# Performance work log

Measured on AMD Instinct MI355X. Metric: run time of the kernel, lower is better.

Reference implementation:

```python
import jax, jax.numpy as jnp
from jax import lax
import numpy as np
import math

MAXV = 127.0  # 2**(8-1)-1, signed int8 narrow range

def setup_inputs() -> dict:
    key = jax.random.key(0)
    kx, kw, kb = jax.random.split(key, 3)
    B, Cin, H, W = 32, 128, 56, 56
    Cout, K = 256, 3
    x = jax.random.normal(kx, (B, Cin, H, W), dtype=jnp.float32)
    # kaiming_uniform_(a=sqrt(5)) -> bound = sqrt(6 / ((1+5) * fan_in)) = 1/sqrt(fan_in)
    fan_in = Cin * K * K
    bound = 1.0 / math.sqrt(fan_in)
    weight = jax.random.uniform(kw, (Cout, Cin, K, K), dtype=jnp.float32,
                                minval=-bound, maxval=bound)
    bias = jax.random.uniform(kb, (Cout,), dtype=jnp.float32,
                              minval=-bound, maxval=bound)
    return {"x": x, "weight": weight, "bias": bias}

def _quantize_i8(t):
    """Max-calibrated signed 8-bit quantization (fake_quant=False -> integer output)."""
    amax = jnp.max(jnp.abs(t))
    scale = MAXV / amax
    q = jnp.clip(jnp.round(t * scale), -MAXV, MAXV).astype(jnp.int8)
    return q, scale

def reference(x, weight, bias):
    # quantize activations and weights to int8
    qx, sx = _quantize_i8(x)
    qw, sw = _quantize_i8(weight)
    # exact int8 conv with int32 accumulation (systolic exact path), stride=1, pad=1
    out_i32 = lax.conv_general_dilated(
        qx, qw,
        window_strides=(1, 1),
        padding=((1, 1), (1, 1)),
        dimension_numbers=("NCHW", "OIHW", "NCHW"),
        preferred_element_type=jnp.int32,
    )
    # dequantize and add bias
    out = out_i32.astype(jnp.float32) / (sx * sw)
    return out + bias[None, :, None, None]
```

## Files before the change

kernel.cpp:

```cpp
#include <hip/hip_runtime.h>


#define B_    32
#define CIN   128
#define H_    56
#define W_    56
#define COUT  256
#define HP    58
#define WP    58
#define HWP   (H_*W_)
#define NPIX  (B_*HWP)
#define NCHUNK 18
#define WCHUNK 16384

typedef int int4v __attribute__((ext_vector_type(4)));

__device__ __forceinline__ void gld_lds16(const void* g, void* l) {
    __builtin_amdgcn_global_load_lds(
        (const __attribute__((address_space(1))) unsigned int*)g,
        (__attribute__((address_space(3))) unsigned int*)l, 16, 0, 0);
}

__global__ __launch_bounds__(256) void amax_kernel(const float4* __restrict__ x, long n4x,
                                                   const float4* __restrict__ wt, long n4w,
                                                   unsigned* __restrict__ scales) {
    const float4* p; long n4; unsigned* slot; long start, stride;
    if (blockIdx.x < 2048) {
        p = x; n4 = n4x; slot = scales;
        start = (long)blockIdx.x * 256 + threadIdx.x; stride = 2048L * 256;
    } else {
        p = wt; n4 = n4w; slot = scales + 1;
        start = (long)(blockIdx.x - 2048) * 256 + threadIdx.x; stride = 128L * 256;
    }
    float m = 0.f;
    for (long i = start; i < n4; i += stride) {
        float4 v = p[i];
        m = fmaxf(m, fmaxf(fmaxf(fabsf(v.x), fabsf(v.y)), fmaxf(fabsf(v.z), fabsf(v.w))));
    }
    __shared__ float red[256];
    red[threadIdx.x] = m; __syncthreads();
    for (int s = 128; s > 0; s >>= 1) {
        if (threadIdx.x < s) red[threadIdx.x] = fmaxf(red[threadIdx.x], red[threadIdx.x + s]);
        __syncthreads();
    }
    if (threadIdx.x == 0) atomicMax(slot, __float_as_uint(red[0]));
}

__global__ __launch_bounds__(256) void quant_x_kernel(const float* __restrict__ x,
        const unsigned* __restrict__ scales, signed char* __restrict__ xq) {
    const int bh = blockIdx.x;
    const int b = bh / H_, h = bh % H_;
    const float sx = 127.0f / __uint_as_float(scales[0]);
    __shared__ int ldsq[W_ * 33];
    const int tid = threadIdx.x;

    int4 z; z.x = 0; z.y = 0; z.z = 0; z.w = 0;
    int4* prow = (int4*)(xq + ((long)b * HP + h + 1) * WP * CIN);
    if (tid < 8) prow[tid] = z;
    else if (tid < 16) prow[456 + tid - 8] = z;
    if (h == 0) {
        int4* r0 = (int4*)(xq + (long)b * HP * WP * CIN);
        for (int i = tid; i < 464; i += 256) r0[i] = z;
    } else if (h == H_ - 1) {
        int4* rt = (int4*)(xq + ((long)b * HP + 57) * WP * CIN);
        for (int i = tid; i < 464; i += 256) rt[i] = z;
    }

    const int w = tid & 63;
    const int chi = tid >> 6;
    if (w < W_) {
        const float* xb = x + (long)b * CIN * HWP + h * W_ + w;
#pragma unroll
        for (int it = 0; it < 8; ++it) {
            const int c4 = it * 4 + chi;
            int pk = 0;
#pragma unroll
            for (int u = 0; u < 4; ++u) {
                float v = xb[(long)(c4 * 4 + u) * HWP];
                float q = fminf(127.f, fmaxf(-127.f, rintf(v * sx)));
                pk |= ((int)q & 0xff) << (u * 8);
            }
            ldsq[w * 33 + c4] = pk;
        }
    }
    __syncthreads();
    int4* dst = (int4*)(xq + (((long)b * HP + h + 1) * WP + 1) * CIN);
    for (int idx = tid; idx < W_ * 8; idx += 256) {
        const int ww = idx >> 3, c16 = idx & 7;
        int4 v;
        v.x = ldsq[ww * 33 + c16 * 4 + 0];
        v.y = ldsq[ww * 33 + c16 * 4 + 1];
        v.z = ldsq[ww * 33 + c16 * 4 + 2];
        v.w = ldsq[ww * 33 + c16 * 4 + 3];
        dst[ww * 8 + c16] = v;
    }
}

__global__ __launch_bounds__(256) void quant_w_kernel(const float* __restrict__ wt,
        const unsigned* __restrict__ scales, signed char* __restrict__ wq) {
    const int id = blockIdx.x * 256 + threadIdx.x;
    if (id >= COUT * 9 * 32) return;
    const float sw = 127.0f / __uint_as_float(scales[1]);
    const int co = id / 288;
    const int r  = id % 288;
    const int t  = r / 32;
    const int c4 = r % 32;
    int pk = 0;
#pragma unroll
    for (int u = 0; u < 4; ++u) {
        float v = wt[(co * CIN + c4 * 4 + u) * 9 + t];
        float q = fminf(127.f, fmaxf(-127.f, rintf(v * sw)));
        pk |= ((int)q & 0xff) << (u * 8);
    }
    const int k = t * CIN + c4 * 4;
    const int chunk = k >> 6;
    const int o = k & 63;
    *(int*)(wq + (long)chunk * WCHUNK + (co >> 7) * 8192 +
            (o >> 4) * 2048 + (co & 127) * 16 + (o & 15)) = pk;
}

__global__ __launch_bounds__(256, 3) void conv_kernel(
        const signed char* __restrict__ xq, const signed char* __restrict__ wq,
        const float* __restrict__ bias, const unsigned* __restrict__ scales,
        float* __restrict__ out) {
    __shared__ signed char smem[24576];

    const int tid = threadIdx.x;
    const int lane = tid & 63;
    const int wv = tid >> 6;
    const int ln = lane & 15;
    const int g  = lane >> 4;

    const int wco2 = wv >> 1;
    const int wpx2 = wv & 1;

    const int bid = blockIdx.x;
    const int wg  = (bid & 7) * 196 + (bid >> 3);
    const int pxt = wg >> 1;
    const int cot = wg & 1;
    const int px_blk = pxt * 128;
    const int cotoff = cot * 8192;

    const int aoff0 = wv * 1024 + lane * 16;
    const int aoff1 = aoff0 + 4096;

    int voff[4];
#pragma unroll
    for (int j = 0; j < 4; ++j) {
        const int pxs = px_blk + wpx2 * 64 + j * 16 + ln;
        const int bS = pxs / HWP, hwS = pxs % HWP;
        const int hS = hwS / W_, wS = hwS % W_;
        voff[j] = ((bS * HP + hS) * WP + wS) * CIN + g * 16;
    }
    const int voff0 = voff[0], voff1 = voff[1], voff2 = voff[2], voff3 = voff[3];

#define STAGE_A(c) { const int bf_ = (c) % 3; \
    gld_lds16(wq + (c) * WCHUNK + cotoff + aoff0, &smem[bf_ * 8192 + aoff0]); \
    gld_lds16(wq + (c) * WCHUNK + cotoff + aoff1, &smem[bf_ * 8192 + aoff1]); }

#define LOADB(c, BN) { const int tap_ = (c) >> 1; \
    const signed char* p_ = xq + ((tap_ / 3) * WP + (tap_ % 3)) * CIN + ((c) & 1) * 64; \
    BN##0 = *(const int4v*)(p_ + voff0); BN##1 = *(const int4v*)(p_ + voff1); \
    BN##2 = *(const int4v*)(p_ + voff2); BN##3 = *(const int4v*)(p_ + voff3); }

#define LDA_(i) (*(const int4v*)&smem[buf * 8192 + g * 2048 + (wco2 * 64 + (i) * 16 + ln) * 16])
#define MM(i, j, A, Bv) acc[i][j] = __builtin_amdgcn_mfma_i32_16x16x64_i8(A, Bv, acc[i][j], 0, 0, 0)

#define CHUNK(c, VM, BC, BN) { \
    const int buf = (c) % 3; \
    asm volatile("s_waitcnt vmcnt(" #VM ")\n\ts_barrier" ::: "memory"); \
    if ((c) + 2 < NCHUNK) STAGE_A((c) + 2); \
    __builtin_amdgcn_sched_barrier(0);   \
    if ((c) + 1 < NCHUNK) LOADB((c) + 1, BN); \
    int4v Af0 = LDA_(0), Af1 = LDA_(1), Af2 = LDA_(2), Af3 = LDA_(3); \
    __builtin_amdgcn_s_setprio(1); \
    MM(0, 0, Af0, BC##0); MM(0, 1, Af0, BC##1); MM(0, 2, Af0, BC##2); MM(0, 3, Af0, BC##3); \
    MM(1, 0, Af1, BC##0); MM(1, 1, Af1, BC##1); MM(1, 2, Af1, BC##2); MM(1, 3, Af1, BC##3); \
    MM(2, 0, Af2, BC##0); MM(2, 1, Af2, BC##1); MM(2, 2, Af2, BC##2); MM(2, 3, Af2, BC##3); \
    MM(3, 0, Af3, BC##0); MM(3, 1, Af3, BC##1); MM(3, 2, Af3, BC##2); MM(3, 3, Af3, BC##3); \
    __builtin_amdgcn_s_setprio(0); }

    int4v acc[4][4] = {};
    int4v Ba0, Ba1, Ba2, Ba3, Bb0, Bb1, Bb2, Bb3;
    STAGE_A(0);
    __builtin_amdgcn_sched_barrier(0);
    STAGE_A(1);
    __builtin_amdgcn_sched_barrier(0);
    LOADB(0, Ba);
    CHUNK(0,  6, Ba, Bb) CHUNK(1,  6, Bb, Ba) CHUNK(2,  6, Ba, Bb) CHUNK(3,  6, Bb, Ba)
    CHUNK(4,  6, Ba, Bb) CHUNK(5,  6, Bb, Ba) CHUNK(6,  6, Ba, Bb) CHUNK(7,  6, Bb, Ba)
    CHUNK(8,  6, Ba, Bb) CHUNK(9,  6, Bb, Ba) CHUNK(10, 6, Ba, Bb) CHUNK(11, 6, Bb, Ba)
    CHUNK(12, 6, Ba, Bb) CHUNK(13, 6, Bb, Ba) CHUNK(14, 6, Ba, Bb) CHUNK(15, 6, Bb, Ba)
    CHUNK(16, 6, Ba, Bb) CHUNK(17, 4, Bb, Ba)
#undef CHUNK
#undef MM
#undef LDA_
#undef LOADB
#undef STAGE_A

    const float ax = __uint_as_float(scales[0]);
    const float aw = __uint_as_float(scales[1]);
    const float inv = 1.0f / ((127.0f / ax) * (127.0f / aw));

    __syncthreads();
    float* ldsT = (float*)smem;

    const int c4 = tid & 31;
    const int rsel = tid >> 5;
    const int px4 = px_blk + c4 * 4;
    const int bb = px4 / HWP, hw = px4 - bb * HWP;
    float* outb = out + ((long)bb * COUT + cot * 128) * HWP + hw;

#pragma unroll
    for (int rnd = 0; rnd < 4; ++rnd) {
        if (wco2 == (rnd >> 1)) {
#pragma unroll
            for (int ii = 0; ii < 2; ++ii) {
                const int i = (rnd & 1) * 2 + ii;
#pragma unroll
                for (int r = 0; r < 4; ++r) {
                    const int cl = ii * 16 + g * 4 + r;
#pragma unroll
                    for (int j = 0; j < 4; ++j)
                        ldsT[cl * 130 + wpx2 * 64 + j * 16 + ln] = (float)acc[i][j][r] * inv;
                }
            }
        }
        __syncthreads();
#pragma unroll
        for (int rr = 0; rr < 4; ++rr) {
            const int row = rr * 8 + rsel;
            const int co = rnd * 32 + row;
            float4 v = *(float4*)&ldsT[row * 130 + c4 * 4];
            const float bsv = bias[cot * 128 + co];
            v.x += bsv; v.y += bsv; v.z += bsv; v.w += bsv;
            *(float4*)&outb[(long)co * HWP] = v;
        }
        if (rnd < 3) __syncthreads();
    }
}

extern "C" void kernel_launch(void* const* d_in, const int* in_sizes, int n_in,
                              void* d_out, int out_size, void* d_ws, size_t ws_size,
                              hipStream_t stream) {
    const float* x  = (const float*)d_in[0];
    const float* wt = (const float*)d_in[1];
    const float* bs = (const float*)d_in[2];
    float* out = (float*)d_out;

    unsigned* scales = (unsigned*)d_ws;
    const size_t XQ_OFF   = 256;
    const size_t XQ_BYTES = (size_t)B_ * HP * WP * CIN;
    signed char* xq = (signed char*)d_ws + XQ_OFF;
    signed char* wq = xq + XQ_BYTES;

    hipMemsetAsync(d_ws, 0, 8, stream);

    const long n4x = (long)B_ * CIN * H_ * W_ / 4;
    const long n4w = (long)COUT * CIN * 9 / 4;
    amax_kernel<<<2176, 256, 0, stream>>>((const float4*)x, n4x, (const float4*)wt, n4w, scales);

    quant_x_kernel<<<B_ * H_, 256, 0, stream>>>(x, scales, xq);
    quant_w_kernel<<<(COUT * 9 * 32 + 255) / 256, 256, 0, stream>>>(wt, scales, wq);

    conv_kernel<<<2 * NPIX / 128, 256, 0, stream>>>(xq, wq, bs, scales, out);
}
```

Before: 240.6 us.

## Stage activation tiles into LDS via async global_load_lds alongside weights

Activation (B operand) fragments are no longer loaded straight from global memory into registers. They are now staged into a triple-buffered LDS region with direct global-to-LDS loads, in the same pipeline as the weight tiles, and read back from LDS per chunk. The goal is to cut duplicated global activation loads across the two waves that share pixels, coalesce the fetches, and free the registers used for double-buffering B. In exchange, LDS use doubles to 48KB, which may limit occupancy at the launch bound of 3 blocks, and each chunk adds LDS reads.

```diff
diff --git a/kernel.cpp b/kernel.cpp
--- a/kernel.cpp
+++ b/kernel.cpp
@@ -123,7 +123,7 @@
         const signed char* __restrict__ xq, const signed char* __restrict__ wq,
         const float* __restrict__ bias, const unsigned* __restrict__ scales,
         float* __restrict__ out) {
-    __shared__ signed char smem[24576];
+    __shared__ signed char smem[49152];
 
     const int tid = threadIdx.x;
     const int lane = tid & 63;
@@ -144,59 +144,52 @@
     const int aoff0 = wv * 1024 + lane * 16;
     const int aoff1 = aoff0 + 4096;
 
-    int voff[4];
-#pragma unroll
-    for (int j = 0; j < 4; ++j) {
-        const int pxs = px_blk + wpx2 * 64 + j * 16 + ln;
-        const int bS = pxs / HWP, hwS = pxs % HWP;
-        const int hS = hwS / W_, wS = hwS % W_;
-        voff[j] = ((bS * HP + hS) * WP + wS) * CIN + g * 16;
-    }
-    const int voff0 = voff[0], voff1 = voff[1], voff2 = voff[2], voff3 = voff[3];
-
-#define STAGE_A(c) { const int bf_ = (c) % 3; \
+    const int px0 = px_blk + lane;
+    const int b0 = px0 / HWP, hw0 = px0 % HWP;
+    const int voffB0 = ((b0 * HP + hw0 / W_) * WP + hw0 % W_) * CIN + wv * 16;
+    const int px1 = px_blk + 64 + lane;
+    const int b1 = px1 / HWP, hw1 = px1 % HWP;
+    const int voffB1 = ((b1 * HP + hw1 / W_) * WP + hw1 % W_) * CIN + wv * 16;
+    const int ldsB0 = wv * 2048 + lane * 16;
+    const int ldsB1 = ldsB0 + 1024;
+
+#define STAGE(c) { const int bf_ = (c) % 3; \
     gld_lds16(wq + (c) * WCHUNK + cotoff + aoff0, &smem[bf_ * 8192 + aoff0]); \
-    gld_lds16(wq + (c) * WCHUNK + cotoff + aoff1, &smem[bf_ * 8192 + aoff1]); }
-
-#define LOADB(c, BN) { const int tap_ = (c) >> 1; \
-    const signed char* p_ = xq + ((tap_ / 3) * WP + (tap_ % 3)) * CIN + ((c) & 1) * 64; \
-    BN##0 = *(const int4v*)(p_ + voff0); BN##1 = *(const int4v*)(p_ + voff1); \
-    BN##2 = *(const int4v*)(p_ + voff2); BN##3 = *(const int4v*)(p_ + voff3); }
+    gld_lds16(wq + (c) * WCHUNK + cotoff + aoff1, &smem[bf_ * 8192 + aoff1]); \
+    const int tap_ = (c) >> 1; \
+    const int toff_ = ((tap_ / 3) * WP + (tap_ % 3)) * CIN + ((c) & 1) * 64; \
+    gld_lds16(xq + toff_ + voffB0, &smem[24576 + bf_ * 8192 + ldsB0]); \
+    gld_lds16(xq + toff_ + voffB1, &smem[24576 + bf_ * 8192 + ldsB1]); }
 
 #define LDA_(i) (*(const int4v*)&smem[buf * 8192 + g * 2048 + (wco2 * 64 + (i) * 16 + ln) * 16])
+#define LDB_(j) (*(const int4v*)&smem[24576 + buf * 8192 + g * 2048 + (wpx2 * 64 + (j) * 16 + ln) * 16])
 #define MM(i, j, A, Bv) acc[i][j] = __builtin_amdgcn_mfma_i32_16x16x64_i8(A, Bv, acc[i][j], 0, 0, 0)
 
-#define CHUNK(c, VM, BC, BN) { \
+#define CHUNK(c, VM) { \
     const int buf = (c) % 3; \
     asm volatile("s_waitcnt vmcnt(" #VM ")\n\ts_barrier" ::: "memory"); \
-    if ((c) + 2 < NCHUNK) STAGE_A((c) + 2); \
-    __builtin_amdgcn_sched_barrier(0);   \
-    if ((c) + 1 < NCHUNK) LOADB((c) + 1, BN); \
+    if ((c) + 2 < NCHUNK) STAGE((c) + 2); \
+    int4v Bf0 = LDB_(0), Bf1 = LDB_(1), Bf2 = LDB_(2), Bf3 = LDB_(3); \
     int4v Af0 = LDA_(0), Af1 = LDA_(1), Af2 = LDA_(2), Af3 = LDA_(3); \
     __builtin_amdgcn_s_setprio(1); \
-    MM(0, 0, Af0, BC##0); MM(0, 1, Af0, BC##1); MM(0, 2, Af0, BC##2); MM(0, 3, Af0, BC##3); \
-    MM(1, 0, Af1, BC##0); MM(1, 1, Af1, BC##1); MM(1, 2, Af1, BC##2); MM(1, 3, Af1, BC##3); \
-    MM(2, 0, Af2, BC##0); MM(2, 1, Af2, BC##1); MM(2, 2, Af2, BC##2); MM(2, 3, Af2, BC##3); \
-    MM(3, 0, Af3, BC##0); MM(3, 1, Af3, BC##1); MM(3, 2, Af3, BC##2); MM(3, 3, Af3, BC##3); \
+    MM(0, 0, Af0, Bf0); MM(0, 1, Af0, Bf1); MM(0, 2, Af0, Bf2); MM(0, 3, Af0, Bf3); \
+    MM(1, 0, Af1, Bf0); MM(1, 1, Af1, Bf1); MM(1, 2, Af1, Bf2); MM(1, 3, Af1, Bf3); \
+    MM(2, 0, Af2, Bf0); MM(2, 1, Af2, Bf1); MM(2, 2, Af2, Bf2); MM(2, 3, Af2, Bf3); \
+    MM(3, 0, Af3, Bf0); MM(3, 1, Af3, Bf1); MM(3, 2, Af3, Bf2); MM(3, 3, Af3, Bf3); \
     __builtin_amdgcn_s_setprio(0); }
 
     int4v acc[4][4] = {};
-    int4v Ba0, Ba1, Ba2, Ba3, Bb0, Bb1, Bb2, Bb3;
-    STAGE_A(0);
+    STAGE(0);
     __builtin_amdgcn_sched_barrier(0);
-    STAGE_A(1);
-    __builtin_amdgcn_sched_barrier(0);
-    LOADB(0, Ba);
-    CHUNK(0,  6, Ba, Bb) CHUNK(1,  6, Bb, Ba) CHUNK(2,  6, Ba, Bb) CHUNK(3,  6, Bb, Ba)
-    CHUNK(4,  6, Ba, Bb) CHUNK(5,  6, Bb, Ba) CHUNK(6,  6, Ba, Bb) CHUNK(7,  6, Bb, Ba)
-    CHUNK(8,  6, Ba, Bb) CHUNK(9,  6, Bb, Ba) CHUNK(10, 6, Ba, Bb) CHUNK(11, 6, Bb, Ba)
-    CHUNK(12, 6, Ba, Bb) CHUNK(13, 6, Bb, Ba) CHUNK(14, 6, Ba, Bb) CHUNK(15, 6, Bb, Ba)
-    CHUNK(16, 6, Ba, Bb) CHUNK(17, 4, Bb, Ba)
+    STAGE(1);
+    CHUNK(0,  4) CHUNK(1,  4) CHUNK(2,  4) CHUNK(3,  4) CHUNK(4,  4) CHUNK(5,  4)
+    CHUNK(6,  4) CHUNK(7,  4) CHUNK(8,  4) CHUNK(9,  4) CHUNK(10, 4) CHUNK(11, 4)
+    CHUNK(12, 4) CHUNK(13, 4) CHUNK(14, 4) CHUNK(15, 4) CHUNK(16, 4) CHUNK(17, 0)
 #undef CHUNK
 #undef MM
 #undef LDA_
-#undef LOADB
-#undef STAGE_A
+#undef LDB_
+#undef STAGE
 
     const float ax = __uint_as_float(scales[0]);
     const float aw = __uint_as_float(scales[1]);
```

Measured after the change: 214.5 us. 10.9% less time.

## Stage padded input row window in LDS and reuse across all conv taps

Applied to the files above, without the earlier changes.

Each block now covers two full output rows of one image (112 pixels) instead of an arbitrary 128-pixel span. Its padded 4x58x128 int8 input window is loaded into LDS once, and B fragments for all 9 taps are read from LDS rather than re-fetched from global memory per chunk. Waves are re-split so each covers 32 output channels by 112 pixels with a 2x7 accumulator tile, and the epilogue is adapted to row-aligned stores. The cost is a larger LDS footprint (about 54KB per block, which puts pressure on the 3-blocks-per-CU target) and an unpipelined prologue load of the window.

```diff
diff --git a/kernel.cpp b/kernel.cpp
--- a/kernel.cpp
+++ b/kernel.cpp
@@ -12,6 +12,8 @@
 #define NPIX  (B_*HWP)
 #define NCHUNK 18
 #define WCHUNK 16384
+#define BWIN  24576
+#define GSTR  3712
 
 typedef int int4v __attribute__((ext_vector_type(4)));
 
@@ -123,7 +125,7 @@
         const signed char* __restrict__ xq, const signed char* __restrict__ wq,
         const float* __restrict__ bias, const unsigned* __restrict__ scales,
         float* __restrict__ out) {
-    __shared__ signed char smem[24576];
+    __shared__ signed char smem[54272];
 
     const int tid = threadIdx.x;
     const int lane = tid & 63;
@@ -131,71 +133,76 @@
     const int ln = lane & 15;
     const int g  = lane >> 4;
 
-    const int wco2 = wv >> 1;
-    const int wpx2 = wv & 1;
-
     const int bid = blockIdx.x;
-    const int wg  = (bid & 7) * 196 + (bid >> 3);
+    const int wg  = (bid & 7) * 224 + (bid >> 3);
     const int pxt = wg >> 1;
     const int cot = wg & 1;
-    const int px_blk = pxt * 128;
+    const int px_blk = pxt * 112;
     const int cotoff = cot * 8192;
+
+    const int b0 = pxt / 28;
+    const int h0 = (pxt % 28) * 2;
 
     const int aoff0 = wv * 1024 + lane * 16;
     const int aoff1 = aoff0 + 4096;
 
-    int voff[4];
-#pragma unroll
-    for (int j = 0; j < 4; ++j) {
-        const int pxs = px_blk + wpx2 * 64 + j * 16 + ln;
-        const int bS = pxs / HWP, hwS = pxs % HWP;
-        const int hS = hwS / W_, wS = hwS % W_;
-        voff[j] = ((bS * HP + hS) * WP + wS) * CIN + g * 16;
-    }
-    const int voff0 = voff[0], voff1 = voff[1], voff2 = voff[2], voff3 = voff[3];
+    int px58v[7];
+#pragma unroll
+    for (int j = 0; j < 7; ++j) {
+        const int pl = j * 16 + ln;
+        px58v[j] = pl + (pl >= 56 ? 2 : 0);
+    }
+
+    const signed char* win = xq + (long)(b0 * HP + h0) * WP * CIN;
+    int4v wbuf[8];
+#pragma unroll
+    for (int k = 0; k < 8; ++k) {
+        const int u = tid + k * 256;
+        if (u < 1856) wbuf[k] = *(const int4v*)(win + u * 16);
+    }
+#pragma unroll
+    for (int k = 0; k < 8; ++k) {
+        const int u = tid + k * 256;
+        if (u < 1856)
+            *(int4v*)&smem[BWIN + (u & 7) * GSTR + (u >> 3) * 16] = wbuf[k];
+    }
 
 #define STAGE_A(c) { const int bf_ = (c) % 3; \
     gld_lds16(wq + (c) * WCHUNK + cotoff + aoff0, &smem[bf_ * 8192 + aoff0]); \
     gld_lds16(wq + (c) * WCHUNK + cotoff + aoff1, &smem[bf_ * 8192 + aoff1]); }
 
-#define LOADB(c, BN) { const int tap_ = (c) >> 1; \
-    const signed char* p_ = xq + ((tap_ / 3) * WP + (tap_ % 3)) * CIN + ((c) & 1) * 64; \
-    BN##0 = *(const int4v*)(p_ + voff0); BN##1 = *(const int4v*)(p_ + voff1); \
-    BN##2 = *(const int4v*)(p_ + voff2); BN##3 = *(const int4v*)(p_ + voff3); }
-
-#define LDA_(i) (*(const int4v*)&smem[buf * 8192 + g * 2048 + (wco2 * 64 + (i) * 16 + ln) * 16])
+    STAGE_A(0);
+    STAGE_A(1);
+    asm volatile("s_waitcnt lgkmcnt(0)" ::: "memory");
+
+#define TAP58(c) ((((c) >> 1) / 3) * 58 + (((c) >> 1) % 3))
+#define LDA_(i) (*(const int4v*)&smem[buf * 8192 + g * 2048 + (wv * 32 + (i) * 16 + ln) * 16])
+#define LDB_(c, j) (*(const int4v*)&smem[BWIN + (((c) & 1) * 4 + g) * GSTR + (px58v[j] + TAP58(c)) * 16])
 #define MM(i, j, A, Bv) acc[i][j] = __builtin_amdgcn_mfma_i32_16x16x64_i8(A, Bv, acc[i][j], 0, 0, 0)
 
-#define CHUNK(c, VM, BC, BN) { \
+#define CHUNK(c, VM) { \
     const int buf = (c) % 3; \
     asm volatile("s_waitcnt vmcnt(" #VM ")\n\ts_barrier" ::: "memory"); \
     if ((c) + 2 < NCHUNK) STAGE_A((c) + 2); \
-    __builtin_amdgcn_sched_barrier(0);   \
-    if ((c) + 1 < NCHUNK) LOADB((c) + 1, BN); \
-    int4v Af0 = LDA_(0), Af1 = LDA_(1), Af2 = LDA_(2), Af3 = LDA_(3); \
+    int4v Bf0 = LDB_(c, 0), Bf1 = LDB_(c, 1), Bf2 = LDB_(c, 2), Bf3 = LDB_(c, 3); \
+    int4v Bf4 = LDB_(c, 4), Bf5 = LDB_(c, 5), Bf6 = LDB_(c, 6); \
+    int4v Af0 = LDA_(0), Af1 = LDA_(1); \
     __builtin_amdgcn_s_setprio(1); \
-    MM(0, 0, Af0, BC##0); MM(0, 1, Af0, BC##1); MM(0, 2, Af0, BC##2); MM(0, 3, Af0, BC##3); \
-    MM(1, 0, Af1, BC##0); MM(1, 1, Af1, BC##1); MM(1, 2, Af1, BC##2); MM(1, 3, Af1, BC##3); \
-    MM(2, 0, Af2, BC##0); MM(2, 1, Af2, BC##1); MM(2, 2, Af2, BC##2); MM(2, 3, Af2, BC##3); \
-    MM(3, 0, Af3, BC##0); MM(3, 1, Af3, BC##1); MM(3, 2, Af3, BC##2); MM(3, 3, Af3, BC##3); \
+    MM(0, 0, Af0, Bf0); MM(1, 0, Af1, Bf0); MM(0, 1, Af0, Bf1); MM(1, 1, Af1, Bf1); \
+    MM(0, 2, Af0, Bf2); MM(1, 2, Af1, Bf2); MM(0, 3, Af0, Bf3); MM(1, 3, Af1, Bf3); \
+    MM(0, 4, Af0, Bf4); MM(1, 4, Af1, Bf4); MM(0, 5, Af0, Bf5); MM(1, 5, Af1, Bf5); \
+    MM(0, 6, Af0, Bf6); MM(1, 6, Af1, Bf6); \
     __builtin_amdgcn_s_setprio(0); }
 
-    int4v acc[4][4] = {};
-    int4v Ba0, Ba1, Ba2, Ba3, Bb0, Bb1, Bb2, Bb3;
-    STAGE_A(0);
-    __builtin_amdgcn_sched_barrier(0);
-    STAGE_A(1);
-    __builtin_amdgcn_sched_barrier(0);
-    LOADB(0, Ba);
-    CHUNK(0,  6, Ba, Bb) CHUNK(1,  6, Bb, Ba) CHUNK(2,  6, Ba, Bb) CHUNK(3,  6, Bb, Ba)
-    CHUNK(4,  6, Ba, Bb) CHUNK(5,  6, Bb, Ba) CHUNK(6,  6, Ba, Bb) CHUNK(7,  6, Bb, Ba)
-    CHUNK(8,  6, Ba, Bb) CHUNK(9,  6, Bb, Ba) CHUNK(10, 6, Ba, Bb) CHUNK(11, 6, Bb, Ba)
-    CHUNK(12, 6, Ba, Bb) CHUNK(13, 6, Bb, Ba) CHUNK(14, 6, Ba, Bb) CHUNK(15, 6, Bb, Ba)
-    CHUNK(16, 6, Ba, Bb) CHUNK(17, 4, Bb, Ba)
+    int4v acc[2][7] = {};
+    CHUNK(0,  2) CHUNK(1,  2) CHUNK(2,  2) CHUNK(3,  2) CHUNK(4,  2) CHUNK(5,  2)
+    CHUNK(6,  2) CHUNK(7,  2) CHUNK(8,  2) CHUNK(9,  2) CHUNK(10, 2) CHUNK(11, 2)
+    CHUNK(12, 2) CHUNK(13, 2) CHUNK(14, 2) CHUNK(15, 2) CHUNK(16, 2) CHUNK(17, 0)
 #undef CHUNK
 #undef MM
+#undef LDB_
 #undef LDA_
-#undef LOADB
+#undef TAP58
 #undef STAGE_A
 
     const float ax = __uint_as_float(scales[0]);
@@ -205,36 +212,31 @@
     __syncthreads();
     float* ldsT = (float*)smem;
 
-    const int c4 = tid & 31;
-    const int rsel = tid >> 5;
-    const int px4 = px_blk + c4 * 4;
-    const int bb = px4 / HWP, hw = px4 - bb * HWP;
-    float* outb = out + ((long)bb * COUT + cot * 128) * HWP + hw;
-
 #pragma unroll
     for (int rnd = 0; rnd < 4; ++rnd) {
-        if (wco2 == (rnd >> 1)) {
-#pragma unroll
-            for (int ii = 0; ii < 2; ++ii) {
-                const int i = (rnd & 1) * 2 + ii;
+        if (wv == rnd) {
+#pragma unroll
+            for (int i = 0; i < 2; ++i)
 #pragma unroll
                 for (int r = 0; r < 4; ++r) {
-                    const int cl = ii * 16 + g * 4 + r;
-#pragma unroll
-                    for (int j = 0; j < 4; ++j)
-                        ldsT[cl * 130 + wpx2 * 64 + j * 16 + ln] = (float)acc[i][j][r] * inv;
+                    const int cl = i * 16 + g * 4 + r;
+#pragma unroll
+                    for (int j = 0; j < 7; ++j)
+                        ldsT[cl * 116 + j * 16 + ln] = (float)acc[i][j][r] * inv;
                 }
-            }
         }
         __syncthreads();
 #pragma unroll
-        for (int rr = 0; rr < 4; ++rr) {
-            const int row = rr * 8 + rsel;
-            const int co = rnd * 32 + row;
-            float4 v = *(float4*)&ldsT[row * 130 + c4 * 4];
-            const float bsv = bias[cot * 128 + co];
-            v.x += bsv; v.y += bsv; v.z += bsv; v.w += bsv;
-            *(float4*)&outb[(long)co * HWP] = v;
+        for (int it = 0; it < 4; ++it) {
+            const int idx = it * 256 + tid;
+            if (idx < 896) {
+                const int row = idx / 28, c4 = idx - row * 28;
+                const int co = cot * 128 + rnd * 32 + row;
+                float4 v = *(float4*)&ldsT[row * 116 + c4 * 4];
+                const float bsv = bias[co];
+                v.x += bsv; v.y += bsv; v.z += bsv; v.w += bsv;
+                *(float4*)&out[((long)b0 * COUT + co) * HWP + h0 * 56 + c4 * 4] = v;
+            }
         }
         if (rnd < 3) __syncthreads();
     }
@@ -263,5 +265,5 @@
     quant_x_kernel<<<B_ * H_, 256, 0, stream>>>(x, scales, xq);
     quant_w_kernel<<<(COUT * 9 * 32 + 255) / 256, 256, 0, stream>>>(wt, scales, wq);
 
-    conv_kernel<<<2 * NPIX / 128, 256, 0, stream>>>(xq, wq, bs, scales, out);
-}
+    conv_kernel<<<2 * NPIX / 112, 256, 0, stream>>>(xq, wq, bs, scales, out);
+}
```

Result: faster. 221.5 us (-7.9%).
